# Kernel optimization log

Hardware: AMD Instinct MI355X
Metric: run time of the kernel (lower is better)

Reference implementation:

```python
import jax, jax.numpy as jnp
import numpy as np

PAD_IDX = 0
B, T, S, H, V = 64, 32, 64, 1024, 32000


def setup_inputs() -> dict:
    key = jax.random.key(0)
    ks = jax.random.split(key, 12)
    s = 0.02
    emb_tbl = jax.random.normal(ks[0], (V, H), jnp.float32) * s
    emb_tbl = emb_tbl.at[PAD_IDX].set(0.0)  # padding_idx row is zero
    return {
        "input": jax.random.randint(ks[1], (B, T), 0, V),
        "memory": jax.random.normal(ks[2], (1, B, H), jnp.float32),
        "encoder_output": jax.random.normal(ks[3], (B, S, H), jnp.float32),
        "xs_len": jax.random.randint(ks[4], (B,), 1, S + 1),
        "embedding": emb_tbl,
        "w_ih": jax.random.normal(ks[5], (3 * H, 2 * H), jnp.float32) * s,
        "w_hh": jax.random.normal(ks[6], (3 * H, H), jnp.float32) * s,
        "b_ih": jnp.zeros((3 * H,), jnp.float32),
        "b_hh": jnp.zeros((3 * H,), jnp.float32),
        "l1": jax.random.normal(ks[7], (H, H), jnp.float32) * s,
        "l2": jax.random.normal(ks[8], (H, 2 * H), jnp.float32) * s,
        "w_out": jax.random.normal(ks[9], (V, H), jnp.float32) * s,
        "b_out": jnp.zeros((V,), jnp.float32),
    }


def _gru_cell(x, h, w_ih, w_hh, b_ih, b_hh):
    # torch.nn.GRUCell math
    gi = x @ w_ih.T + b_ih          # [B, 3H]
    gh = h @ w_hh.T + b_hh          # [B, 3H]
    ir, iz, inn = jnp.split(gi, 3, axis=1)
    hr, hz, hn = jnp.split(gh, 3, axis=1)
    r = jax.nn.sigmoid(ir + hr)
    z = jax.nn.sigmoid(iz + hz)
    n = jnp.tanh(inn + r * hn)
    return (1.0 - z) * n + z * h


def _attention(hidden, enc, seq_mask, l1, l2):
    # hidden: [B,H], enc: [B,S,H], seq_mask: [B,S] float {0,1}
    q = hidden @ l1.T                              # [B,H]
    score = jnp.einsum("bsh,bh->bs", enc, q)       # [B,S]
    masked = seq_mask * score
    # faithful to `masked_att[masked_att == 0] = -1e10`
    masked = jnp.where(masked == 0.0, -1e10, masked)
    attn = jax.nn.softmax(masked, axis=1)          # softmax over source positions
    ctx = jnp.einsum("bs,bsh->bh", attn, enc)      # [B,H]
    out = jnp.tanh(jnp.concatenate([ctx, hidden], axis=1) @ l2.T)
    return out, attn


def reference(input, memory, encoder_output, xs_len, embedding,
              w_ih, w_hh, b_ih, b_hh, l1, l2, w_out, b_out):
    emb = embedding[input]                         # [B,T,H]
    emb_t = jnp.swapaxes(emb, 0, 1)                # [T,B,H]
    h0 = memory[0]                                 # [B,H]
    ctx0 = jnp.zeros_like(h0)
    s_len = encoder_output.shape[1]
    seq_mask = (jnp.arange(s_len)[None, :] < xs_len[:, None]).astype(emb.dtype)  # [B,S]

    def step(carry, e_t):
        h_prev, ctx = carry
        x = jnp.concatenate([e_t, ctx], axis=1)    # [B,2H]
        h = _gru_cell(x, h_prev, w_ih, w_hh, b_ih, b_hh)
        ctx_new, attn = _attention(h, encoder_output, seq_mask, l1, l2)
        scores = jax.nn.log_softmax(ctx_new @ w_out.T + b_out, axis=1)  # [B,V]
        return (h, ctx_new), (scores, attn)

    (h_fin, ctx_fin), (all_scores, all_attn) = jax.lax.scan(step, (h0, ctx0), emb_t)
    decoder_output = jnp.swapaxes(all_scores, 0, 1)        # [B,T,V]
    decoder_hidden = h_fin[None, :, :]                     # [1,B,H]
    attention_weights = jnp.swapaxes(all_attn, 0, 1)       # [B,T,S]
    return decoder_output, decoder_hidden, attention_weights, ctx_fin
```

## Files before the change

kernel.cpp:

```cpp
#include <hip/hip_runtime.h>


#define B_ 64
#define T_ 32
#define S_ 64
#define H_ 1024
#define V_ 32000
#define NB_ 256
#define LDS_BYTES 152064

#define HID_OFF 65536000L
#define ATT_OFF 65601536L
#define CTF_OFF 65732608L

typedef __attribute__((ext_vector_type(8))) short bf16x8;
typedef __attribute__((ext_vector_type(4))) float f32x4;
typedef __attribute__((ext_vector_type(4))) unsigned int u32x4;
typedef unsigned short u16;
typedef unsigned long long u64;

__device__ __forceinline__ u16 f2bf(float v) {
  unsigned int u = __float_as_uint(v);
  unsigned int r = (u + 0x7fffu + ((u >> 16) & 1u)) >> 16;
  return (u16)r;
}
__device__ __forceinline__ float bf2f(u16 h) {
  return __uint_as_float(((unsigned int)h) << 16);
}
__device__ __forceinline__ void split2(float v, u16* hi, u16* lo) {
  u16 h = f2bf(v);
  *hi = h;
  *lo = f2bf(v - bf2f(h));
}

__device__ __forceinline__ u64 aload_u64(const void* p) {
  return __hip_atomic_load((const u64*)p, __ATOMIC_RELAXED, __HIP_MEMORY_SCOPE_AGENT);
}
__device__ __forceinline__ unsigned aload_u32(const void* p) {
  return __hip_atomic_load((const unsigned*)p, __ATOMIC_RELAXED, __HIP_MEMORY_SCOPE_AGENT);
}
__device__ __forceinline__ void astore_u64(void* p, u64 v) {
  __hip_atomic_store((u64*)p, v, __ATOMIC_RELAXED, __HIP_MEMORY_SCOPE_AGENT);
}
__device__ __forceinline__ void astore_f32(float* p, float v) {
  __hip_atomic_store((unsigned*)p, __float_as_uint(v), __ATOMIC_RELAXED,
                     __HIP_MEMORY_SCOPE_AGENT);
}

__device__ __forceinline__ void gll16(const u16* g, u16* l) {
  __builtin_amdgcn_global_load_lds(
      (const __attribute__((address_space(1))) void*)g,
      (__attribute__((address_space(3))) void*)l, 16, 0, 0);
}


__global__ void k_split4(const float* __restrict__ sA, u16* __restrict__ hA,
                         u16* __restrict__ lA, int nA,
                         const float* __restrict__ sB, u16* __restrict__ hB,
                         u16* __restrict__ lB, int nB,
                         const float* __restrict__ sC, u16* __restrict__ hC,
                         u16* __restrict__ lC, int nC,
                         const float* __restrict__ sD, u16* __restrict__ hD,
                         u16* __restrict__ lD, int nD) {
  int i = blockIdx.x * blockDim.x + threadIdx.x;
  int stride = gridDim.x * blockDim.x;
  int t1 = nA, t2 = nA + nB, t3 = t2 + nC, total = t3 + nD;
  for (; i < total; i += stride) {
    if (i < t1) split2(sA[i], &hA[i], &lA[i]);
    else if (i < t2) { int j = i - t1; split2(sB[j], &hB[j], &lB[j]); }
    else if (i < t3) { int j = i - t2; split2(sC[j], &hC[j], &lC[j]); }
    else { int j = i - t3; split2(sD[j], &hD[j], &lD[j]); }
  }
}

__global__ void k_tobf(const float* __restrict__ src, u16* __restrict__ dst, int n) {
  int i = blockIdx.x * blockDim.x + threadIdx.x;
  int stride = gridDim.x * blockDim.x;
  for (; i < n; i += stride) dst[i] = f2bf(src[i]);
}

__global__ void k_l1t(const float* __restrict__ l1, u16* __restrict__ hi,
                      u16* __restrict__ lo) {
  __shared__ float tile[64][65];
  int it = blockIdx.x & 15, kt = blockIdx.x >> 4;
  for (int q = 0; q < 16; ++q) {
    int idx = q * 256 + threadIdx.x;
    int r = idx >> 6, c = idx & 63;
    tile[r][c] = l1[(long)(it * 64 + r) * H_ + kt * 64 + c];
  }
  __syncthreads();
  for (int q = 0; q < 16; ++q) {
    int idx = q * 256 + threadIdx.x;
    int r = idx >> 6, c = idx & 63;
    long o = (long)(kt * 64 + r) * H_ + it * 64 + c;
    split2(tile[c][r], &hi[o], &lo[o]);
  }
}

__global__ void k_embx(const int* __restrict__ inp, const float* __restrict__ emb,
                       u16* __restrict__ hi, u16* __restrict__ lo) {
  int bt = blockIdx.x;
  int b = bt >> 5, t = bt & 31;
  int id = inp[b * T_ + t];
  const float* src = emb + (long)id * H_;
  long base = (long)(t * B_ + b) * H_;
  for (int k = threadIdx.x; k < H_; k += 256) split2(src[k], &hi[base + k], &lo[base + k]);
}

__global__ void k_h0(const float* __restrict__ mem, u16* __restrict__ hh,
                     u16* __restrict__ hl) {
  int i = blockIdx.x * 256 + threadIdx.x;
  float v = mem[i];
  split2(v, &hh[i], &hl[i]);
}

__global__ void k_guard(float* out, float v) {
  if (blockIdx.x == 0 && threadIdx.x == 0) out[0] = v;
}

template <int SPLIT>
__launch_bounds__(256)
__global__ void k_gemm128(const u16* __restrict__ Ah, const u16* __restrict__ Al,
                          const u16* __restrict__ Bh, const u16* __restrict__ Bl,
                          float* __restrict__ C, int Mtiles, int K, int Arow,
                          int Brow, int Crow) {
  int bx = blockIdx.x;
  int mt = bx % Mtiles, nt = bx / Mtiles;
  int m0 = mt * 128, n0 = nt * 128;

  __shared__ __attribute__((aligned(16))) u16 lds[(SPLIT ? 4 : 2) * 4096];
  char* L = (char*)lds;
  const int tid = threadIdx.x;
  const int lane = tid & 63, wid = tid >> 6;
  const int wm = wid & 1, wn = wid >> 1;
  const int l15 = lane & 15, kq = lane >> 4;

  f32x4 acc[4][4];
  const f32x4 z4 = {0.f, 0.f, 0.f, 0.f};
#pragma unroll
  for (int i = 0; i < 4; ++i)
#pragma unroll
    for (int j = 0; j < 4; ++j) acc[i][j] = z4;

  const int ksteps = K >> 5;
  for (int kt = 0; kt < ksteps; ++kt) {
    __syncthreads();
#pragma unroll
    for (int h2 = 0; h2 < 2; ++h2) {
      int r = (tid >> 2) + (h2 << 6);
      int slot = tid & 3;
      int so = ((slot ^ (r & 3)) << 4);
      long ga = (long)(m0 + r) * Arow + (kt << 5) + (slot << 3);
      long gb = (long)(n0 + r) * Brow + (kt << 5) + (slot << 3);
      *(u32x4*)(L + r * 64 + so) = *(const u32x4*)(Ah + ga);
      *(u32x4*)(L + 8192 + r * 64 + so) = *(const u32x4*)(Bh + gb);
      if (SPLIT) {
        *(u32x4*)(L + 16384 + r * 64 + so) = *(const u32x4*)(Al + ga);
        *(u32x4*)(L + 24576 + r * 64 + so) = *(const u32x4*)(Bl + gb);
      }
    }
    __syncthreads();
    bf16x8 aH[4], bH[4], aL[4], bL[4];
#pragma unroll
    for (int mi = 0; mi < 4; ++mi) {
      int r = (wm << 6) + (mi << 4) + l15;
      int off = r * 64 + ((kq ^ (r & 3)) << 4);
      aH[mi] = *(const bf16x8*)(L + off);
      if (SPLIT) aL[mi] = *(const bf16x8*)(L + 16384 + off);
    }
#pragma unroll
    for (int ni = 0; ni < 4; ++ni) {
      int c = (wn << 6) + (ni << 4) + l15;
      int off = c * 64 + ((kq ^ (c & 3)) << 4);
      bH[ni] = *(const bf16x8*)(L + 8192 + off);
      if (SPLIT) bL[ni] = *(const bf16x8*)(L + 24576 + off);
    }
#pragma unroll
    for (int mi = 0; mi < 4; ++mi)
#pragma unroll
      for (int ni = 0; ni < 4; ++ni) {
        acc[mi][ni] = __builtin_amdgcn_mfma_f32_16x16x32_bf16(aH[mi], bH[ni], acc[mi][ni], 0, 0, 0);
        if (SPLIT) {
          acc[mi][ni] = __builtin_amdgcn_mfma_f32_16x16x32_bf16(aL[mi], bH[ni], acc[mi][ni], 0, 0, 0);
          acc[mi][ni] = __builtin_amdgcn_mfma_f32_16x16x32_bf16(aH[mi], bL[ni], acc[mi][ni], 0, 0, 0);
        }
      }
  }
#pragma unroll
  for (int mi = 0; mi < 4; ++mi)
#pragma unroll
    for (int ni = 0; ni < 4; ++ni)
#pragma unroll
      for (int e = 0; e < 4; ++e) {
        int r = (wm << 6) + (mi << 4) + (kq << 2) + e;
        int c = (wn << 6) + (ni << 4) + l15;
        C[(long)(m0 + r) * Crow + n0 + c] = acc[mi][ni][e];
      }
}

__launch_bounds__(256)
__global__ void k_gemmL(const u16* __restrict__ A, const u16* __restrict__ Bw,
                        const float* __restrict__ bias, float* __restrict__ C) {
  int bx = blockIdx.x;
  int wg = (bx & 7) * 500 + (bx >> 3);
  int mt = wg & 15, nt = wg >> 4;
  int m0 = mt << 7, n0 = nt << 7;

  __shared__ __attribute__((aligned(16))) u16 lds[2 * 4096];
  char* L = (char*)lds;
  const int tid = threadIdx.x;
  const int lane = tid & 63, wid = tid >> 6;
  const int wm = wid & 1, wn = wid >> 1;
  const int l15 = lane & 15, kq = lane >> 4;

  const int r8 = lane >> 2, ss = lane & 3;
  const int rA0 = (wid << 4) + r8, rA1 = rA0 + 64;
  const u16* gA0 = A + (long)(m0 + rA0) * 1024 + ((ss ^ (rA0 & 3)) << 3);
  const u16* gA1 = A + (long)(m0 + rA1) * 1024 + ((ss ^ (rA1 & 3)) << 3);
  const u16* gB0 = Bw + (long)(n0 + rA0) * 1024 + ((ss ^ (rA0 & 3)) << 3);
  const u16* gB1 = Bw + (long)(n0 + rA1) * 1024 + ((ss ^ (rA1 & 3)) << 3);
  u16* lA0 = (u16*)(L + (wid << 10));
  u16* lA1 = (u16*)(L + 4096 + (wid << 10));
  u16* lB0 = (u16*)(L + 8192 + (wid << 10));
  u16* lB1 = (u16*)(L + 12288 + (wid << 10));

  f32x4 acc[4][4];
  const f32x4 z4 = {0.f, 0.f, 0.f, 0.f};
#pragma unroll
  for (int i = 0; i < 4; ++i)
#pragma unroll
    for (int j = 0; j < 4; ++j) acc[i][j] = z4;

  for (int kt = 0; kt < 32; ++kt) {
    __syncthreads();
    gll16(gA0 + (kt << 5), lA0);
    gll16(gA1 + (kt << 5), lA1);
    gll16(gB0 + (kt << 5), lB0);
    gll16(gB1 + (kt << 5), lB1);
    __syncthreads();
    bf16x8 aF[4], bF[4];
#pragma unroll
    for (int mi = 0; mi < 4; ++mi) {
      int r = (wm << 6) + (mi << 4) + l15;
      aF[mi] = *(const bf16x8*)(L + r * 64 + ((kq ^ (r & 3)) << 4));
    }
#pragma unroll
    for (int ni = 0; ni < 4; ++ni) {
      int c = (wn << 6) + (ni << 4) + l15;
      bF[ni] = *(const bf16x8*)(L + 8192 + c * 64 + ((kq ^ (c & 3)) << 4));
    }
#pragma unroll
    for (int mi = 0; mi < 4; ++mi)
#pragma unroll
      for (int ni = 0; ni < 4; ++ni)
        acc[mi][ni] = __builtin_amdgcn_mfma_f32_16x16x32_bf16(aF[mi], bF[ni], acc[mi][ni], 0, 0, 0);
  }
#pragma unroll
  for (int mi = 0; mi < 4; ++mi)
#pragma unroll
    for (int ni = 0; ni < 4; ++ni)
#pragma unroll
      for (int e = 0; e < 4; ++e) {
        int r = (wm << 6) + (mi << 4) + (kq << 2) + e;
        int c = (wn << 6) + (ni << 4) + l15;
        int gm = m0 + r, gn = n0 + c;
        float v = acc[mi][ni][e] + bias[gn];
        C[((long)(gm & 63) * T_ + (gm >> 6)) * V_ + gn] = v;
      }
}

__device__ __forceinline__ void gridbar(unsigned* flags, unsigned seq) {
  __syncthreads();
  if (threadIdx.x == 0)
    __hip_atomic_store(flags + blockIdx.x * 16, seq, __ATOMIC_RELEASE,
                       __HIP_MEMORY_SCOPE_AGENT);
  if (threadIdx.x < 64) {
    int l = threadIdx.x;
    for (;;) {
      unsigned a = __hip_atomic_load(flags + l * 16, __ATOMIC_RELAXED, __HIP_MEMORY_SCOPE_AGENT);
      unsigned b = __hip_atomic_load(flags + (l + 64) * 16, __ATOMIC_RELAXED, __HIP_MEMORY_SCOPE_AGENT);
      unsigned c = __hip_atomic_load(flags + (l + 128) * 16, __ATOMIC_RELAXED, __HIP_MEMORY_SCOPE_AGENT);
      unsigned d = __hip_atomic_load(flags + (l + 192) * 16, __ATOMIC_RELAXED, __HIP_MEMORY_SCOPE_AGENT);
      if (__all((a >= seq) & (b >= seq) & (c >= seq) & (d >= seq))) break;
      __builtin_amdgcn_s_sleep(1);
    }
  }
  __syncthreads();
}

__launch_bounds__(256)
__global__ void k_rec(const float* __restrict__ embi,
                      u16* __restrict__ dctx_h, u16* __restrict__ dctx_l,
                      u16* __restrict__ hh_r, u16* __restrict__ hl_r,
                      const float* __restrict__ memory,
                      const u16* __restrict__ wih_h, const u16* __restrict__ wih_l,
                      const u16* __restrict__ whh_h, const u16* __restrict__ whh_l,
                      const u16* __restrict__ l2_h, const u16* __restrict__ l2_l,
                      float* __restrict__ gip, float* __restrict__ ghp,
                      float* __restrict__ psc, float* __restrict__ ctxp,
                      const float* __restrict__ encT, const float* __restrict__ encL,
                      const int* __restrict__ xs_len,
                      const float* __restrict__ bih, const float* __restrict__ bhh,
                      float* __restrict__ dout, unsigned* flags) {
  extern __shared__ __attribute__((aligned(16))) char L[];
  char* W_HI = L;
  char* W_LO = L + 65536;
  char* A_HI = L + 131072;
  char* A_LO = L + 139264;
  float* hq = (float*)(L + 147456);
  float* at_s = (float*)(L + 148480);
  const int bx = blockIdx.x;
  const int tid = threadIdx.x;
  const int lane = tid & 63, wid = tid >> 6;
  const int wm = wid & 1, wn = wid >> 1;
  const int l15 = lane & 15, kq = lane >> 4;
  const f32x4 z4 = {0.f, 0.f, 0.f, 0.f};
  unsigned seq = 1;

  const int isGI = (bx < 96);
  const int isGH = (bx >= 96 && bx < 192);
  const int isL2 = (bx >= 192 && bx < 224);
  const int sb = bx >> 2;
  const int sq = bx & 3;
  int nt = 0, kc = 0, n0 = 0;
  const u16 *Wg_h = nullptr, *Wg_l = nullptr;
  int wrs = 0;
  if (isGI) {
    nt = bx % 48; kc = bx / 48;
    Wg_h = wih_h + 1024 + (long)nt * 64 * 2048 + kc * 512;
    Wg_l = wih_l + 1024 + (long)nt * 64 * 2048 + kc * 512;
    wrs = 2048;
  } else if (isGH) {
    int j2 = bx - 96;
    nt = j2 % 48; kc = j2 / 48;
    Wg_h = whh_h + (long)nt * 64 * 1024 + kc * 512;
    Wg_l = whh_l + (long)nt * 64 * 1024 + kc * 512;
    wrs = 1024;
  } else if (isL2) {
    n0 = (bx - 192) << 5;
    Wg_h = l2_h + 1024 + (long)n0 * 2048;
    Wg_l = l2_l + 1024 + (long)n0 * 2048;
    wrs = 2048;
  }

  if (isGI || isGH) {
    for (int e = tid; e < 4096; e += 256) {
      int st = e >> 8, r = (e >> 2) & 63, slot = e & 3;
      long g = (long)r * wrs + st * 32 + slot * 8;
      int o = st * 4096 + r * 64 + ((slot ^ (r & 3)) << 4);
      *(u32x4*)(W_HI + o) = *(const u32x4*)(Wg_h + g);
      *(u32x4*)(W_LO + o) = *(const u32x4*)(Wg_l + g);
    }
  } else if (isL2) {
    for (int e = tid; e < 4096; e += 256) {
      int st = e >> 7, r = (e >> 2) & 31, slot = e & 3;
      long g = (long)r * wrs + st * 32 + slot * 8;
      int o = st * 2048 + r * 64 + ((slot ^ (r & 3)) << 4);
      *(u32x4*)(W_HI + o) = *(const u32x4*)(Wg_h + g);
      *(u32x4*)(W_LO + o) = *(const u32x4*)(Wg_l + g);
    }
  }
  __syncthreads();

  float hpv = memory[sb * 1024 + sq * 256 + tid];

  const int pr = tid >> 2, ps = tid & 3;
  const int ao = pr * 64 + ((ps ^ (pr & 3)) << 4);

  for (int t = 0; t < T_; ++t) {
    if (isGI || isGH) {
      const u16* Ah;
      const u16* Al;
      float* outp;
      if (isGI) {
        Ah = dctx_h + (long)t * 65536 + kc * 512;
        Al = dctx_l + (long)t * 65536 + kc * 512;
        outp = gip + (long)kc * 196608 + nt * 64;
      } else {
        Ah = hh_r + (long)t * 65536 + kc * 512;
        Al = hl_r + (long)t * 65536 + kc * 512;
        outp = ghp + (long)kc * 196608 + nt * 64;
      }
      const long g0 = (long)pr * 1024 + ps * 8;
      u32x4 ph0 = *(const u32x4*)(Ah + g0);
      u32x4 ph1 = *(const u32x4*)(Ah + g0 + 32);
      u32x4 pl0 = *(const u32x4*)(Al + g0);
      u32x4 pl1 = *(const u32x4*)(Al + g0 + 32);

      f32x4 acc[2][2];
#pragma unroll
      for (int i = 0; i < 2; ++i)
#pragma unroll
        for (int j = 0; j < 2; ++j) acc[i][j] = z4;

      for (int kt = 0; kt < 8; ++kt) {
        __syncthreads();
        *(u32x4*)(A_HI + ao) = ph0;
        *(u32x4*)(A_HI + 4096 + ao) = ph1;
        *(u32x4*)(A_LO + ao) = pl0;
        *(u32x4*)(A_LO + 4096 + ao) = pl1;
        __syncthreads();
        if (kt < 7) {
          long g = g0 + (kt + 1) * 64;
          ph0 = *(const u32x4*)(Ah + g);
          ph1 = *(const u32x4*)(Ah + g + 32);
          pl0 = *(const u32x4*)(Al + g);
          pl1 = *(const u32x4*)(Al + g + 32);
        }
#pragma unroll
        for (int sub = 0; sub < 2; ++sub) {
          const int stw = (kt * 2 + sub) * 4096;
          const int sta = sub * 4096;
          bf16x8 aH[2], aL[2], bH[2], bL[2];
#pragma unroll
          for (int mi = 0; mi < 2; ++mi) {
            int rr = (wm << 5) + (mi << 4) + l15;
            int off = rr * 64 + ((kq ^ (rr & 3)) << 4);
            aH[mi] = *(const bf16x8*)(A_HI + sta + off);
            aL[mi] = *(const bf16x8*)(A_LO + sta + off);
          }
#pragma unroll
          for (int ni = 0; ni < 2; ++ni) {
            int c = (wn << 5) + (ni << 4) + l15;
            int off = c * 64 + ((kq ^ (c & 3)) << 4);
            bH[ni] = *(const bf16x8*)(W_HI + stw + off);
            bL[ni] = *(const bf16x8*)(W_LO + stw + off);
          }
#pragma unroll
          for (int mi = 0; mi < 2; ++mi)
#pragma unroll
            for (int ni = 0; ni < 2; ++ni) {
              acc[mi][ni] = __builtin_amdgcn_mfma_f32_16x16x32_bf16(aH[mi], bH[ni], acc[mi][ni], 0, 0, 0);
              acc[mi][ni] = __builtin_amdgcn_mfma_f32_16x16x32_bf16(aL[mi], bH[ni], acc[mi][ni], 0, 0, 0);
              acc[mi][ni] = __builtin_amdgcn_mfma_f32_16x16x32_bf16(aH[mi], bL[ni], acc[mi][ni], 0, 0, 0);
            }
        }
      }
#pragma unroll
      for (int mi = 0; mi < 2; ++mi)
#pragma unroll
        for (int ni = 0; ni < 2; ++ni)
#pragma unroll
          for (int e = 0; e < 4; ++e) {
            int r = (wm << 5) + (mi << 4) + (kq << 2) + e;
            int c = (wn << 5) + (ni << 4) + l15;
            astore_f32(outp + (long)r * 3072 + c, acc[mi][ni][e]);
          }
    }
    gridbar(flags, seq); seq++;

    {
      const int b = sb, q = sq;
      const int j = (q << 8) + tid;
      const float* eb = embi + ((long)t * 64 + b) * 3072;
      float g0r = __uint_as_float(aload_u32(gip + b * 3072 + j));
      float g1r = __uint_as_float(aload_u32(gip + 196608 + b * 3072 + j));
      float g0z = __uint_as_float(aload_u32(gip + b * 3072 + 1024 + j));
      float g1z = __uint_as_float(aload_u32(gip + 196608 + b * 3072 + 1024 + j));
      float g0n = __uint_as_float(aload_u32(gip + b * 3072 + 2048 + j));
      float g1n = __uint_as_float(aload_u32(gip + 196608 + b * 3072 + 2048 + j));
      float h0r = __uint_as_float(aload_u32(ghp + b * 3072 + j));
      float h1r = __uint_as_float(aload_u32(ghp + 196608 + b * 3072 + j));
      float h0z = __uint_as_float(aload_u32(ghp + b * 3072 + 1024 + j));
      float h1z = __uint_as_float(aload_u32(ghp + 196608 + b * 3072 + 1024 + j));
      float h0n = __uint_as_float(aload_u32(ghp + b * 3072 + 2048 + j));
      float h1n = __uint_as_float(aload_u32(ghp + 196608 + b * 3072 + 2048 + j));
      float ir = eb[j] + g0r + g1r + bih[j];
      float iz = eb[1024 + j] + g0z + g1z + bih[1024 + j];
      float in2 = eb[2048 + j] + g0n + g1n + bih[2048 + j];
      float hr = h0r + h1r + bhh[j];
      float hz = h0z + h1z + bhh[1024 + j];
      float hn = h0n + h1n + bhh[2048 + j];
      float r = 1.f / (1.f + expf(-(ir + hr)));
      float z = 1.f / (1.f + expf(-(iz + hz)));
      float n = tanhf(in2 + r * hn);
      float h = (1.f - z) * n + z * hpv;
      hpv = h;
      hq[tid] = h;
      if (t == T_ - 1) dout[HID_OFF + (long)b * 1024 + j] = h;
      __syncthreads();
      if (tid < 64) {
        u64 ph = 0, pl = 0;
#pragma unroll
        for (int ii = 0; ii < 4; ++ii) {
          u16 hi, lo;
          split2(hq[tid * 4 + ii], &hi, &lo);
          ph |= (u64)hi << (16 * ii);
          pl |= (u64)lo << (16 * ii);
        }
        long o = (long)(t + 1) * 65536 + (long)b * 1024 + (q << 8) + tid * 4;
        astore_u64(hh_r + o, ph);
        astore_u64(hl_r + o, pl);
      }
      {
        int s = tid >> 2, part = tid & 3;
        const float4* ep = (const float4*)(encT + (((long)b * 64 + s) << 10) + (q << 8) + (part << 6));
        const float4* hp = (const float4*)(hq + (part << 6));
        float dot = 0.f;
#pragma unroll
        for (int kk = 0; kk < 16; ++kk) {
          float4 e = ep[kk], a = hp[kk];
          dot += e.x * a.x + e.y * a.y + e.z * a.z + e.w * a.w;
        }
        dot += __shfl_xor(dot, 1);
        dot += __shfl_xor(dot, 2);
        if (part == 0) astore_f32(psc + (((b << 2) + q) << 6) + s, dot);
      }
    }
    gridbar(flags, seq); seq++;

    {
      const int b = sb, q = sq;
      if (tid < 64) {
        int s = tid;
        float v = 0.f;
#pragma unroll
        for (int qq = 0; qq < 4; ++qq)
          v += __uint_as_float(aload_u32(psc + (((b << 2) + qq) << 6) + s));
        int len = xs_len[b];
        if (s >= len || v == 0.0f) v = -1e10f;
        float m = v;
#pragma unroll
        for (int off = 32; off; off >>= 1) m = fmaxf(m, __shfl_xor(m, off));
        float p = expf(v - m);
        float sum = p;
#pragma unroll
        for (int off = 32; off; off >>= 1) sum += __shfl_xor(sum, off);
        float a = p / sum;
        at_s[s] = a;
        if (q == 0) dout[ATT_OFF + ((long)b * T_ + t) * S_ + s] = a;
      }
      __syncthreads();
      {
        const float* lp = encL + (((long)b * 64 + (q << 4)) << 10) + tid * 4;
        float c0 = 0.f, c1 = 0.f, c2 = 0.f, c3 = 0.f;
#pragma unroll
        for (int s2 = 0; s2 < 16; ++s2) {
          float a = at_s[(q << 4) + s2];
          float4 e = *(const float4*)(lp + (s2 << 10));
          c0 += a * e.x; c1 += a * e.y; c2 += a * e.z; c3 += a * e.w;
        }
        u64 w0 = ((u64)__float_as_uint(c1) << 32) | __float_as_uint(c0);
        u64 w1 = ((u64)__float_as_uint(c3) << 32) | __float_as_uint(c2);
        long o = (((long)(b << 2) + q) << 10) + tid * 4;
        astore_u64(ctxp + o, w0);
        astore_u64(ctxp + o + 2, w1);
      }
    }
    gridbar(flags, seq); seq++;

    if (isL2) {
      const u16* Ah = hh_r + (long)(t + 1) * 65536;
      const u16* Al = hl_r + (long)(t + 1) * 65536;
      const long g0 = (long)pr * 1024 + ps * 8;
      u32x4 ph0 = *(const u32x4*)(Ah + g0);
      u32x4 ph1 = *(const u32x4*)(Ah + g0 + 32);
      u32x4 pl0 = *(const u32x4*)(Al + g0);
      u32x4 pl1 = *(const u32x4*)(Al + g0 + 32);

      f32x4 acc[2];
      acc[0] = z4; acc[1] = z4;
      for (int kt = 0; kt < 16; ++kt) {
        __syncthreads();
        *(u32x4*)(A_HI + ao) = ph0;
        *(u32x4*)(A_HI + 4096 + ao) = ph1;
        *(u32x4*)(A_LO + ao) = pl0;
        *(u32x4*)(A_LO + 4096 + ao) = pl1;
        __syncthreads();
        if (kt < 15) {
          long g = g0 + (kt + 1) * 64;
          ph0 = *(const u32x4*)(Ah + g);
          ph1 = *(const u32x4*)(Ah + g + 32);
          pl0 = *(const u32x4*)(Al + g);
          pl1 = *(const u32x4*)(Al + g + 32);
        }
#pragma unroll
        for (int sub = 0; sub < 2; ++sub) {
          const int stw = (kt * 2 + sub) * 2048;
          const int sta = sub * 4096;
          bf16x8 aH[2], aL[2], bH, bL;
#pragma unroll
          for (int mi = 0; mi < 2; ++mi) {
            int rr = (wm << 5) + (mi << 4) + l15;
            int off = rr * 64 + ((kq ^ (rr & 3)) << 4);
            aH[mi] = *(const bf16x8*)(A_HI + sta + off);
            aL[mi] = *(const bf16x8*)(A_LO + sta + off);
          }
          {
            int c = (wn << 4) + l15;
            int off = c * 64 + ((kq ^ (c & 3)) << 4);
            bH = *(const bf16x8*)(W_HI + stw + off);
            bL = *(const bf16x8*)(W_LO + stw + off);
          }
#pragma unroll
          for (int mi = 0; mi < 2; ++mi) {
            acc[mi] = __builtin_amdgcn_mfma_f32_16x16x32_bf16(aH[mi], bH, acc[mi], 0, 0, 0);
            acc[mi] = __builtin_amdgcn_mfma_f32_16x16x32_bf16(aL[mi], bH, acc[mi], 0, 0, 0);
            acc[mi] = __builtin_amdgcn_mfma_f32_16x16x32_bf16(aH[mi], bL, acc[mi], 0, 0, 0);
          }
        }
      }
      __syncthreads();
      float* cf = (float*)(L + 131072);
#pragma unroll
      for (int mi = 0; mi < 2; ++mi)
#pragma unroll
        for (int e = 0; e < 4; ++e) {
          int rr = (wm << 5) + (mi << 4) + (kq << 2) + e;
          int cc = (wn << 4) + l15;
          float a = 0.f;
#pragma unroll
          for (int qq = 0; qq < 4; ++qq)
            a += __uint_as_float(aload_u32(ctxp + (((long)(rr << 2) + qq) << 10) + n0 + cc));
          float v = tanhf(acc[mi][e] + a);
          if (t == T_ - 1) dout[CTF_OFF + (long)rr * 1024 + n0 + cc] = v;
          cf[rr * 32 + cc] = v;
        }
      __syncthreads();
#pragma unroll
      for (int qq2 = 0; qq2 < 2; ++qq2) {
        int g = tid + qq2 * 256;
        int b = g >> 3, colg = g & 7;
        u64 ph = 0, pl = 0;
#pragma unroll
        for (int ii = 0; ii < 4; ++ii) {
          float v = cf[b * 32 + colg * 4 + ii];
          u16 hi, lo;
          split2(v, &hi, &lo);
          ph |= (u64)hi << (16 * ii);
          pl |= (u64)lo << (16 * ii);
        }
        long o = (long)(t + 1) * 65536 + (long)b * 1024 + n0 + colg * 4;
        astore_u64(dctx_h + o, ph);
        astore_u64(dctx_l + o, pl);
      }
    }
    if (t < T_ - 1) { gridbar(flags, seq); }
    seq++;
  }
}

__device__ __forceinline__ void lse_comb(float& m, float& s, float mo, float so) {
  float M = fmaxf(m, mo);
  s = s * __expf(m - M) + so * __expf(mo - M);
  m = M;
}
__device__ __forceinline__ void lse_push(float& m, float& s, float x) {
  if (x > m) {
    s = s * __expf(m - x) + 1.f;
    m = x;
  } else {
    s += __expf(x - m);
  }
}

__launch_bounds__(256)
__global__ void k_lsm(float* __restrict__ dout) {
  long base = (long)blockIdx.x * V_;
  int tid = threadIdx.x;
  float m = -3.0e38f, s = 0.f;
  const float4* p4 = (const float4*)(dout + base);
#pragma unroll 4
  for (int it = 0; it < 31; ++it) {
    float4 x = p4[it * 256 + tid];
    lse_push(m, s, x.x); lse_push(m, s, x.y);
    lse_push(m, s, x.z); lse_push(m, s, x.w);
  }
  if (tid < 64) {
    float4 x = p4[7936 + tid];
    lse_push(m, s, x.x); lse_push(m, s, x.y);
    lse_push(m, s, x.z); lse_push(m, s, x.w);
  }
#pragma unroll
  for (int off = 32; off; off >>= 1) {
    float mo = __shfl_xor(m, off), so = __shfl_xor(s, off);
    lse_comb(m, s, mo, so);
  }
  __shared__ float ms[4], ss[4];
  if ((tid & 63) == 0) { ms[tid >> 6] = m; ss[tid >> 6] = s; }
  __syncthreads();
  float M = ms[0], S = ss[0];
  for (int w2 = 1; w2 < 4; ++w2) lse_comb(M, S, ms[w2], ss[w2]);
  float logden = M + logf(S);
  float4* q4 = (float4*)(dout + base);
#pragma unroll 4
  for (int it = 0; it < 31; ++it) {
    float4 x = q4[it * 256 + tid];
    x.x -= logden; x.y -= logden; x.z -= logden; x.w -= logden;
    q4[it * 256 + tid] = x;
  }
  if (tid < 64) {
    float4 x = q4[7936 + tid];
    x.x -= logden; x.y -= logden; x.z -= logden; x.w -= logden;
    q4[7936 + tid] = x;
  }
}

extern "C" void kernel_launch(void* const* d_in, const int* in_sizes, int n_in,
                              void* d_out, int out_size, void* d_ws, size_t ws_size,
                              hipStream_t stream) {
  (void)in_sizes; (void)n_in; (void)out_size;
  const int* input = (const int*)d_in[0];
  const float* memory = (const float*)d_in[1];
  const float* enc = (const float*)d_in[2];
  const int* xs_len = (const int*)d_in[3];
  const float* emb = (const float*)d_in[4];
  const float* wih = (const float*)d_in[5];
  const float* whh = (const float*)d_in[6];
  const float* bih = (const float*)d_in[7];
  const float* bhh = (const float*)d_in[8];
  const float* l1 = (const float*)d_in[9];
  const float* l2 = (const float*)d_in[10];
  const float* wout = (const float*)d_in[11];
  const float* bout = (const float*)d_in[12];
  float* out = (float*)d_out;
  char* w = (char*)d_ws;

  size_t off = 0;
  auto alloc = [&](size_t bytes) {
    size_t o = off;
    off = (off + bytes + 255) & ~(size_t)255;
    return o;
  };
  const size_t N_WIH = 3072UL * 2048, N_WHH = 3072UL * 1024, N_L2 = 1024UL * 2048;
  const size_t N_L1 = 1024UL * 1024, N_ENC = 4096UL * 1024, N_WOUT = 32000UL * 1024;
  const size_t N_EMBX = 2048UL * 1024, N_ENCT = 4096UL * 1024;
  const size_t N_EMBI = 2048UL * 3072, N_ROT = 33UL * 65536;

  size_t o_wih_h = alloc(2 * N_WIH), o_wih_l = alloc(2 * N_WIH);
  size_t o_whh_h = alloc(2 * N_WHH), o_whh_l = alloc(2 * N_WHH);
  size_t o_l2_h = alloc(2 * N_L2), o_l2_l = alloc(2 * N_L2);
  size_t o_l1t_h = alloc(2 * N_L1), o_l1t_l = alloc(2 * N_L1);
  size_t o_ctx_h = alloc(2 * N_ROT), o_ctx_l = alloc(2 * N_ROT);
  size_t o_hh = alloc(2 * N_ROT), o_hl = alloc(2 * N_ROT);
  size_t o_gip = alloc(4 * 2 * 196608), o_ghp = alloc(4 * 2 * 196608);
  size_t o_psc = alloc(4 * 16384);
  size_t o_ctxp = alloc(4 * 262144);
  size_t o_bar = alloc(16384);
  size_t o_arena = alloc(2 * N_ENC * 2 + 2 * N_EMBX * 2 + 4 * N_EMBI + 4 * N_ENCT * 2);

  if (off > ws_size) {
    k_guard<<<1, 1, 0, stream>>>(out, 1.0e8f + (float)(ws_size >> 20));
    return;
  }

  u16* wih_h = (u16*)(w + o_wih_h);   u16* wih_l = (u16*)(w + o_wih_l);
  u16* whh_h = (u16*)(w + o_whh_h);   u16* whh_l = (u16*)(w + o_whh_l);
  u16* l2_h = (u16*)(w + o_l2_h);     u16* l2_l = (u16*)(w + o_l2_l);
  u16* l1t_h = (u16*)(w + o_l1t_h);   u16* l1t_l = (u16*)(w + o_l1t_l);
  u16* ctx_h = (u16*)(w + o_ctx_h);   u16* ctx_l = (u16*)(w + o_ctx_l);
  u16* hh_r = (u16*)(w + o_hh);       u16* hl_r = (u16*)(w + o_hl);
  float* gip = (float*)(w + o_gip);
  float* ghp = (float*)(w + o_ghp);
  float* psc = (float*)(w + o_psc);
  float* ctxp = (float*)(w + o_ctxp);
  unsigned* flags = (unsigned*)(w + o_bar);

  char* ar = w + o_arena;
  u16* enc_h = (u16*)ar;
  u16* enc_l = (u16*)(ar + 2 * N_ENC);
  u16* embx_h = (u16*)(ar + 4 * N_ENC);
  u16* embx_l = (u16*)(ar + 4 * N_ENC + 2 * N_EMBX);
  float* embi = (float*)(ar + 4 * N_ENC + 4 * N_EMBX);
  float* encT = (float*)(ar + 4 * N_ENC + 4 * N_EMBX + 4 * N_EMBI);
  float* encL = (float*)(ar + 4 * N_ENC + 4 * N_EMBX + 4 * N_EMBI + 4 * N_ENCT);
  u16* wout_b = (u16*)ar;

  hipFuncSetAttribute((const void*)k_rec, hipFuncAttributeMaxDynamicSharedMemorySize,
                      LDS_BYTES);

  k_split4<<<4096, 256, 0, stream>>>(wih, wih_h, wih_l, (int)N_WIH,
                                     whh, whh_h, whh_l, (int)N_WHH,
                                     l2, l2_h, l2_l, (int)N_L2,
                                     enc, enc_h, enc_l, (int)N_ENC);
  k_l1t<<<256, 256, 0, stream>>>(l1, l1t_h, l1t_l);
  k_embx<<<2048, 256, 0, stream>>>(input, emb, embx_h, embx_l);
  k_h0<<<256, 256, 0, stream>>>(memory, hh_r, hl_r);
  hipMemsetAsync(ctx_h, 0, 131072, stream);
  hipMemsetAsync(ctx_l, 0, 131072, stream);
  hipMemsetAsync(flags, 0, 16384, stream);

  k_gemm128<1><<<256, 256, 0, stream>>>(enc_h, enc_l, l1t_h, l1t_l, encT,
                                        32, 1024, 1024, 1024, 1024);
  k_gemm128<1><<<256, 256, 0, stream>>>(enc_h, enc_l, l2_h, l2_l, encL,
                                        32, 1024, 1024, 2048, 1024);
  k_gemm128<1><<<384, 256, 0, stream>>>(embx_h, embx_l, wih_h, wih_l, embi,
                                        16, 1024, 1024, 2048, 3072);

  k_rec<<<NB_, 256, LDS_BYTES, stream>>>(embi, ctx_h, ctx_l, hh_r, hl_r, memory,
                                         wih_h, wih_l, whh_h, whh_l, l2_h, l2_l,
                                         gip, ghp, psc, ctxp, encT, encL,
                                         xs_len, bih, bhh, out, flags);

  k_tobf<<<4096, 256, 0, stream>>>(wout, wout_b, (int)N_WOUT);

  k_gemmL<<<4000, 256, 0, stream>>>(ctx_h + 65536, wout_b, bout, out);

  k_lsm<<<2048, 256, 0, stream>>>(out);
}
```

Before: 1.960 ms.

## Fuse log-softmax partial reductions into output GEMM epilogue; use direct-to-LDS loads in precompute GEMMs

The vocabulary GEMM epilogue now computes per-row max and sum-of-exp partials for each 128-column tile and writes them to a small workspace. The log-softmax kernel merges 250 partials instead of re-reading the full 32000-wide logits row, which removes one full pass over the output. The split-bf16 precompute GEMMs are specialised to K=1024 and switched to per-wave global-to-LDS loads via gll16. In exchange the GEMM epilogue gains shuffles and exp work, and a partial-sum buffer is added.

```diff
diff --git a/kernel.cpp b/kernel.cpp
--- a/kernel.cpp
+++ b/kernel.cpp
@@ -118,23 +118,42 @@
   if (blockIdx.x == 0 && threadIdx.x == 0) out[0] = v;
 }
 
-template <int SPLIT>
 __launch_bounds__(256)
-__global__ void k_gemm128(const u16* __restrict__ Ah, const u16* __restrict__ Al,
-                          const u16* __restrict__ Bh, const u16* __restrict__ Bl,
-                          float* __restrict__ C, int Mtiles, int K, int Arow,
-                          int Brow, int Crow) {
+__global__ void k_gemmG(const u16* __restrict__ Ah, const u16* __restrict__ Al,
+                        const u16* __restrict__ Bh, const u16* __restrict__ Bl,
+                        float* __restrict__ C, int Mtiles, int Arow, int Brow,
+                        int Crow) {
   int bx = blockIdx.x;
   int mt = bx % Mtiles, nt = bx / Mtiles;
-  int m0 = mt * 128, n0 = nt * 128;
-
-  __shared__ __attribute__((aligned(16))) u16 lds[(SPLIT ? 4 : 2) * 4096];
+  int m0 = mt << 7, n0 = nt << 7;
+
+  __shared__ __attribute__((aligned(16))) u16 lds[4 * 4096];
   char* L = (char*)lds;
   const int tid = threadIdx.x;
   const int lane = tid & 63, wid = tid >> 6;
   const int wm = wid & 1, wn = wid >> 1;
   const int l15 = lane & 15, kq = lane >> 4;
 
+  const int r8 = lane >> 2, ss = lane & 3;
+  const int rA0 = (wid << 4) + r8, rA1 = rA0 + 64;
+  const int sw0 = (ss ^ (rA0 & 3)) << 3, sw1 = (ss ^ (rA1 & 3)) << 3;
+  const u16* gAh0 = Ah + (long)(m0 + rA0) * Arow + sw0;
+  const u16* gAh1 = Ah + (long)(m0 + rA1) * Arow + sw1;
+  const u16* gAl0 = Al + (long)(m0 + rA0) * Arow + sw0;
+  const u16* gAl1 = Al + (long)(m0 + rA1) * Arow + sw1;
+  const u16* gBh0 = Bh + (long)(n0 + rA0) * Brow + sw0;
+  const u16* gBh1 = Bh + (long)(n0 + rA1) * Brow + sw1;
+  const u16* gBl0 = Bl + (long)(n0 + rA0) * Brow + sw0;
+  const u16* gBl1 = Bl + (long)(n0 + rA1) * Brow + sw1;
+  u16* dAh0 = (u16*)(L + (wid << 10));
+  u16* dAh1 = (u16*)(L + 4096 + (wid << 10));
+  u16* dBh0 = (u16*)(L + 8192 + (wid << 10));
+  u16* dBh1 = (u16*)(L + 12288 + (wid << 10));
+  u16* dAl0 = (u16*)(L + 16384 + (wid << 10));
+  u16* dAl1 = (u16*)(L + 20480 + (wid << 10));
+  u16* dBl0 = (u16*)(L + 24576 + (wid << 10));
+  u16* dBl1 = (u16*)(L + 28672 + (wid << 10));
+
   f32x4 acc[4][4];
   const f32x4 z4 = {0.f, 0.f, 0.f, 0.f};
 #pragma unroll
@@ -142,23 +161,17 @@
 #pragma unroll
     for (int j = 0; j < 4; ++j) acc[i][j] = z4;
 
-  const int ksteps = K >> 5;
-  for (int kt = 0; kt < ksteps; ++kt) {
+  for (int kt = 0; kt < 32; ++kt) {
     __syncthreads();
-#pragma unroll
-    for (int h2 = 0; h2 < 2; ++h2) {
-      int r = (tid >> 2) + (h2 << 6);
-      int slot = tid & 3;
-      int so = ((slot ^ (r & 3)) << 4);
-      long ga = (long)(m0 + r) * Arow + (kt << 5) + (slot << 3);
-      long gb = (long)(n0 + r) * Brow + (kt << 5) + (slot << 3);
-      *(u32x4*)(L + r * 64 + so) = *(const u32x4*)(Ah + ga);
-      *(u32x4*)(L + 8192 + r * 64 + so) = *(const u32x4*)(Bh + gb);
-      if (SPLIT) {
-        *(u32x4*)(L + 16384 + r * 64 + so) = *(const u32x4*)(Al + ga);
-        *(u32x4*)(L + 24576 + r * 64 + so) = *(const u32x4*)(Bl + gb);
-      }
-    }
+    int ko = kt << 5;
+    gll16(gAh0 + ko, dAh0);
+    gll16(gAh1 + ko, dAh1);
+    gll16(gBh0 + ko, dBh0);
+    gll16(gBh1 + ko, dBh1);
+    gll16(gAl0 + ko, dAl0);
+    gll16(gAl1 + ko, dAl1);
+    gll16(gBl0 + ko, dBl0);
+    gll16(gBl1 + ko, dBl1);
     __syncthreads();
     bf16x8 aH[4], bH[4], aL[4], bL[4];
 #pragma unroll
@@ -166,24 +179,22 @@
       int r = (wm << 6) + (mi << 4) + l15;
       int off = r * 64 + ((kq ^ (r & 3)) << 4);
       aH[mi] = *(const bf16x8*)(L + off);
-      if (SPLIT) aL[mi] = *(const bf16x8*)(L + 16384 + off);
+      aL[mi] = *(const bf16x8*)(L + 16384 + off);
     }
 #pragma unroll
     for (int ni = 0; ni < 4; ++ni) {
       int c = (wn << 6) + (ni << 4) + l15;
       int off = c * 64 + ((kq ^ (c & 3)) << 4);
       bH[ni] = *(const bf16x8*)(L + 8192 + off);
-      if (SPLIT) bL[ni] = *(const bf16x8*)(L + 24576 + off);
+      bL[ni] = *(const bf16x8*)(L + 24576 + off);
     }
 #pragma unroll
     for (int mi = 0; mi < 4; ++mi)
 #pragma unroll
       for (int ni = 0; ni < 4; ++ni) {
         acc[mi][ni] = __builtin_amdgcn_mfma_f32_16x16x32_bf16(aH[mi], bH[ni], acc[mi][ni], 0, 0, 0);
-        if (SPLIT) {
-          acc[mi][ni] = __builtin_amdgcn_mfma_f32_16x16x32_bf16(aL[mi], bH[ni], acc[mi][ni], 0, 0, 0);
-          acc[mi][ni] = __builtin_amdgcn_mfma_f32_16x16x32_bf16(aH[mi], bL[ni], acc[mi][ni], 0, 0, 0);
-        }
+        acc[mi][ni] = __builtin_amdgcn_mfma_f32_16x16x32_bf16(aL[mi], bH[ni], acc[mi][ni], 0, 0, 0);
+        acc[mi][ni] = __builtin_amdgcn_mfma_f32_16x16x32_bf16(aH[mi], bL[ni], acc[mi][ni], 0, 0, 0);
       }
   }
 #pragma unroll
@@ -198,15 +209,23 @@
       }
 }
 
+__device__ __forceinline__ void lse_comb(float& m, float& s, float mo, float so) {
+  float M = fmaxf(m, mo);
+  s = s * __expf(m - M) + so * __expf(mo - M);
+  m = M;
+}
+
 __launch_bounds__(256)
 __global__ void k_gemmL(const u16* __restrict__ A, const u16* __restrict__ Bw,
-                        const float* __restrict__ bias, float* __restrict__ C) {
+                        const float* __restrict__ bias, float* __restrict__ C,
+                        float2* __restrict__ psum) {
   int bx = blockIdx.x;
   int wg = (bx & 7) * 500 + (bx >> 3);
   int mt = wg & 15, nt = wg >> 4;
   int m0 = mt << 7, n0 = nt << 7;
 
   __shared__ __attribute__((aligned(16))) u16 lds[2 * 4096];
+  __shared__ float2 lsep[128][2];
   char* L = (char*)lds;
   const int tid = threadIdx.x;
   const int lane = tid & 63, wid = tid >> 6;
@@ -255,18 +274,41 @@
       for (int ni = 0; ni < 4; ++ni)
         acc[mi][ni] = __builtin_amdgcn_mfma_f32_16x16x32_bf16(aF[mi], bF[ni], acc[mi][ni], 0, 0, 0);
   }
+  float b4[4];
+#pragma unroll
+  for (int ni = 0; ni < 4; ++ni) b4[ni] = bias[n0 + (wn << 6) + (ni << 4) + l15];
 #pragma unroll
   for (int mi = 0; mi < 4; ++mi)
 #pragma unroll
-    for (int ni = 0; ni < 4; ++ni)
-#pragma unroll
-      for (int e = 0; e < 4; ++e) {
-        int r = (wm << 6) + (mi << 4) + (kq << 2) + e;
-        int c = (wn << 6) + (ni << 4) + l15;
-        int gm = m0 + r, gn = n0 + c;
-        float v = acc[mi][ni][e] + bias[gn];
-        C[((long)(gm & 63) * T_ + (gm >> 6)) * V_ + gn] = v;
-      }
+    for (int e = 0; e < 4; ++e) {
+      int r = (wm << 6) + (mi << 4) + (kq << 2) + e;
+      int gm = m0 + r;
+      float vv[4], vm = -3.0e38f, vs = 0.f;
+#pragma unroll
+      for (int ni = 0; ni < 4; ++ni) {
+        vv[ni] = acc[mi][ni][e] + b4[ni];
+        vm = fmaxf(vm, vv[ni]);
+      }
+#pragma unroll
+      for (int ni = 0; ni < 4; ++ni) {
+        vs += __expf(vv[ni] - vm);
+        int gn = n0 + (wn << 6) + (ni << 4) + l15;
+        C[((long)(gm & 63) * T_ + (gm >> 6)) * V_ + gn] = vv[ni];
+      }
+#pragma unroll
+      for (int o = 1; o < 16; o <<= 1) {
+        float mo = __shfl_xor(vm, o), so = __shfl_xor(vs, o);
+        lse_comb(vm, vs, mo, so);
+      }
+      if (l15 == 0) lsep[r][wn] = make_float2(vm, vs);
+    }
+  __syncthreads();
+  if (tid < 128) {
+    float2 a = lsep[tid][0], b2 = lsep[tid][1];
+    float M = a.x, S = a.y;
+    lse_comb(M, S, b2.x, b2.y);
+    psum[((long)(m0 + tid) << 8) + nt] = make_float2(M, S);
+  }
 }
 
 __device__ __forceinline__ void gridbar(unsigned* flags, unsigned seq) {
@@ -640,36 +682,18 @@
   }
 }
 
-__device__ __forceinline__ void lse_comb(float& m, float& s, float mo, float so) {
-  float M = fmaxf(m, mo);
-  s = s * __expf(m - M) + so * __expf(mo - M);
-  m = M;
-}
-__device__ __forceinline__ void lse_push(float& m, float& s, float x) {
-  if (x > m) {
-    s = s * __expf(m - x) + 1.f;
-    m = x;
-  } else {
-    s += __expf(x - m);
-  }
-}
-
 __launch_bounds__(256)
-__global__ void k_lsm(float* __restrict__ dout) {
-  long base = (long)blockIdx.x * V_;
+__global__ void k_lsm(float* __restrict__ dout, const float2* __restrict__ psum) {
+  int R = blockIdx.x;
+  long base = (long)R * V_;
+  int gm = ((R & 31) << 6) + (R >> 5);
+  const float2* pp = psum + ((long)gm << 8);
   int tid = threadIdx.x;
   float m = -3.0e38f, s = 0.f;
-  const float4* p4 = (const float4*)(dout + base);
-#pragma unroll 4
-  for (int it = 0; it < 31; ++it) {
-    float4 x = p4[it * 256 + tid];
-    lse_push(m, s, x.x); lse_push(m, s, x.y);
-    lse_push(m, s, x.z); lse_push(m, s, x.w);
-  }
-  if (tid < 64) {
-    float4 x = p4[7936 + tid];
-    lse_push(m, s, x.x); lse_push(m, s, x.y);
-    lse_push(m, s, x.z); lse_push(m, s, x.w);
+  if (tid < 250) {
+    float2 p = pp[tid];
+    m = p.x;
+    s = p.y;
   }
 #pragma unroll
   for (int off = 32; off; off >>= 1) {
@@ -736,6 +760,7 @@
   size_t o_gip = alloc(4 * 2 * 196608), o_ghp = alloc(4 * 2 * 196608);
   size_t o_psc = alloc(4 * 16384);
   size_t o_ctxp = alloc(4 * 262144);
+  size_t o_psum = alloc(8UL * 2048 * 256);
   size_t o_bar = alloc(16384);
   size_t o_arena = alloc(2 * N_ENC * 2 + 2 * N_EMBX * 2 + 4 * N_EMBI + 4 * N_ENCT * 2);
 
@@ -754,6 +779,7 @@
   float* ghp = (float*)(w + o_ghp);
   float* psc = (float*)(w + o_psc);
   float* ctxp = (float*)(w + o_ctxp);
+  float2* psum = (float2*)(w + o_psum);
   unsigned* flags = (unsigned*)(w + o_bar);
 
   char* ar = w + o_arena;
@@ -780,12 +806,12 @@
   hipMemsetAsync(ctx_l, 0, 131072, stream);
   hipMemsetAsync(flags, 0, 16384, stream);
 
-  k_gemm128<1><<<256, 256, 0, stream>>>(enc_h, enc_l, l1t_h, l1t_l, encT,
-                                        32, 1024, 1024, 1024, 1024);
-  k_gemm128<1><<<256, 256, 0, stream>>>(enc_h, enc_l, l2_h, l2_l, encL,
-                                        32, 1024, 1024, 2048, 1024);
-  k_gemm128<1><<<384, 256, 0, stream>>>(embx_h, embx_l, wih_h, wih_l, embi,
-                                        16, 1024, 1024, 2048, 3072);
+  k_gemmG<<<256, 256, 0, stream>>>(enc_h, enc_l, l1t_h, l1t_l, encT,
+                                   32, 1024, 1024, 1024);
+  k_gemmG<<<256, 256, 0, stream>>>(enc_h, enc_l, l2_h, l2_l, encL,
+                                   32, 1024, 2048, 1024);
+  k_gemmG<<<384, 256, 0, stream>>>(embx_h, embx_l, wih_h, wih_l, embi,
+                                   16, 1024, 2048, 3072);
 
   k_rec<<<NB_, 256, LDS_BYTES, stream>>>(embi, ctx_h, ctx_l, hh_r, hl_r, memory,
                                          wih_h, wih_l, whh_h, whh_l, l2_h, l2_l,
@@ -794,7 +820,7 @@
 
   k_tobf<<<4096, 256, 0, stream>>>(wout, wout_b, (int)N_WOUT);
 
-  k_gemmL<<<4000, 256, 0, stream>>>(ctx_h + 65536, wout_b, bout, out);
-
-  k_lsm<<<2048, 256, 0, stream>>>(out);
-}
+  k_gemmL<<<4000, 256, 0, stream>>>(ctx_h + 65536, wout_b, bout, out, psum);
+
+  k_lsm<<<2048, 256, 0, stream>>>(out, psum);
+}
```

After: 1.948 ms, median of 2. Within noise of the previous version (-0.6%).
